# Optimization experiments

Measured on AMD Instinct MI355X. Metric: run time of the kernel, lower is better.

## Reference

```python
import jax, jax.numpy as jnp
import numpy as np

LN_EPS = 1e-5

def _ln(x, w, b):
    mu = jnp.mean(x, axis=-1, keepdims=True)
    var = jnp.var(x, axis=-1, keepdims=True)
    return (x - mu) * jax.lax.rsqrt(var + LN_EPS) * w + b

def setup_inputs() -> dict:
    key = jax.random.key(0)
    ks = jax.random.split(key, 16)
    B, T, N = 32, 1024, 77
    D, TD, TE = 512, 256, 2048
    s = lambda fan: 1.0 / np.sqrt(fan)
    return {
        "x": jax.random.normal(ks[0], (B, T, D), jnp.float32),
        "xf": jax.random.normal(ks[1], (B, N, TD), jnp.float32),
        "emb": jax.random.normal(ks[2], (B, TE), jnp.float32),
        "src_mask": jnp.ones((B, T), jnp.float32),
        "cond_type": jax.random.randint(ks[3], (B,), 0, 100, jnp.int64),
        "norm_w": jnp.ones((D,), jnp.float32),
        "norm_b": jnp.zeros((D,), jnp.float32),
        "tnorm_w": jnp.ones((TD,), jnp.float32),
        "tnorm_b": jnp.zeros((TD,), jnp.float32),
        "Wq": jax.random.normal(ks[4], (D, D), jnp.float32) * s(D),
        "bq": jnp.zeros((D,), jnp.float32),
        "Wk": jax.random.normal(ks[5], (D, TD), jnp.float32) * s(TD),
        "bk": jnp.zeros((D,), jnp.float32),
        "Wv": jax.random.normal(ks[6], (D, TD), jnp.float32) * s(TD),
        "bv": jnp.zeros((D,), jnp.float32),
        "emb_w": jax.random.normal(ks[7], (2 * D, TE), jnp.float32) * s(TE),
        "emb_b": jnp.zeros((2 * D,), jnp.float32),
        "snorm_w": jnp.ones((D,), jnp.float32),
        "snorm_b": jnp.zeros((D,), jnp.float32),
        "Wout": jax.random.normal(ks[8], (D, D), jnp.float32) * s(D),
        "bout": jnp.zeros((D,), jnp.float32),
    }

def reference(x, xf, emb, src_mask, cond_type,
              norm_w, norm_b, tnorm_w, tnorm_b,
              Wq, bq, Wk, bk, Wv, bv,
              emb_w, emb_b, snorm_w, snorm_b, Wout, bout):
    B, T, D = x.shape
    N = xf.shape[1]
    H = 8
    dh = D // H
    # projections (no 1/sqrt(dh) scaling, per original)
    q = (_ln(x, norm_w, norm_b) @ Wq.T + bq).reshape(B, T, H, dh)
    xf_n = _ln(xf, tnorm_w, tnorm_b)
    k = (xf_n @ Wk.T + bk).reshape(B, N, H, dh)
    # cond_type gating: text_cond_type = (cond_type % 10 > 0)
    tc = (cond_type % 10 > 0).astype(x.dtype)  # [B]
    bias = (1.0 - tc)[:, None, None, None] * -1000000.0  # [B,1,1,1]
    attn = jnp.einsum('bthd,bnhd->btnh', q, k) + bias
    attn = jax.nn.softmax(attn, axis=2)  # over keys N
    v = (xf_n @ Wv.T + bv) * tc[:, None, None]
    v = v.reshape(B, N, H, dh)
    y = jnp.einsum('btnh,bnhd->bthd', attn, v).reshape(B, T, D)
    # StylizationBlock: silu->linear on emb -> scale/shift, ln, silu->linear, residual
    e = jax.nn.silu(emb) @ emb_w.T + emb_b  # [B, 2D]
    scale, shift = jnp.split(e[:, None, :], 2, axis=2)  # [B,1,D] each
    h = _ln(y, snorm_w, snorm_b) * (1.0 + scale) + shift
    h = jax.nn.silu(h) @ Wout.T + bout
    return x + h
```

## Files before the change

kernel.cpp:

```cpp
#include <hip/hip_runtime.h>
#include <math.h>

#define B_   32
#define T_   1024
#define N_   77
#define D_   512
#define TD_  256
#define TE_  2048
#define H_   8
#define DH_  64

typedef short bf16x8 __attribute__((ext_vector_type(8)));
typedef float f32x4  __attribute__((ext_vector_type(4)));

__device__ __forceinline__ float sigmoidf_fast(float x) {
    return 1.0f / (1.0f + __expf(-x));
}

__device__ __forceinline__ unsigned short f2b(float f) {
    unsigned int u = __float_as_uint(f);
    unsigned int r = u + 0x7FFFu + ((u >> 16) & 1u);
    return (unsigned short)(r >> 16);
}

__device__ __forceinline__ float b2f(short us) {
    return __uint_as_float(((unsigned int)(unsigned short)us) << 16);
}

#define GL16(g, l) __builtin_amdgcn_global_load_lds(                         \
    (const __attribute__((address_space(1))) unsigned int*)(g),              \
    (__attribute__((address_space(3))) unsigned int*)(l), 16, 0, 0)

#define WAITV8() asm volatile("s_waitcnt vmcnt(8)" ::: "memory")
#define WAITV4() asm volatile("s_waitcnt vmcnt(4)" ::: "memory")
#define WAITV0() asm volatile("s_waitcnt vmcnt(0)" ::: "memory")
#define WAITL0() asm volatile("s_waitcnt lgkmcnt(0)" ::: "memory")
#define SBAR()   __builtin_amdgcn_s_barrier()
#define SCHED0() __builtin_amdgcn_sched_barrier(0)

__global__ __launch_bounds__(256) void ln_xf_kernel(
    const float* __restrict__ x, const float* __restrict__ w, const float* __restrict__ b,
    unsigned short* __restrict__ outb)
{
    int row = blockIdx.x * 4 + (threadIdx.x >> 6);
    int lane = threadIdx.x & 63;
    const float* rp = x + (size_t)row * TD_ + lane * 4;
    float4 v = *(const float4*)rp;
    float s  = v.x + v.y + v.z + v.w;
    float ss = v.x*v.x + v.y*v.y + v.z*v.z + v.w*v.w;
    #pragma unroll
    for (int off = 32; off; off >>= 1) {
        s  += __shfl_xor(s, off);
        ss += __shfl_xor(ss, off);
    }
    float m = s * (1.f / TD_);
    float r = rsqrtf(ss * (1.f / TD_) - m * m + 1e-5f);
    float4 wv = *(const float4*)(w + lane * 4);
    float4 bv = *(const float4*)(b + lane * 4);
    ushort4 o;
    o.x = f2b((v.x - m) * r * wv.x + bv.x);
    o.y = f2b((v.y - m) * r * wv.y + bv.y);
    o.z = f2b((v.z - m) * r * wv.z + bv.z);
    o.w = f2b((v.w - m) * r * wv.w + bv.w);
    *(ushort4*)(outb + (size_t)row * TD_ + lane * 4) = o;
}

__global__ __launch_bounds__(256) void conv_weights_kernel(
    const float* __restrict__ Wq, const float* __restrict__ Wout,
    const float* __restrict__ Wk, const float* __restrict__ Wv,
    unsigned short* __restrict__ wqb, unsigned short* __restrict__ wob,
    unsigned short* __restrict__ wkvb)
{
    int bid = blockIdx.x;
    const float* src; unsigned short* dst;
    if (bid < 128)      { src = Wq;   dst = wqb; }
    else if (bid < 256) { src = Wout; dst = wob;               bid -= 128; }
    else if (bid < 320) { src = Wk;   dst = wkvb;              bid -= 256; }
    else                { src = Wv;   dst = wkvb + D_ * TD_;   bid -= 320; }
    int idx = (bid * 256 + threadIdx.x) * 8;
    float4 v0 = *(const float4*)(src + idx);
    float4 v1 = *(const float4*)(src + idx + 4);
    ushort4 o0 = {f2b(v0.x), f2b(v0.y), f2b(v0.z), f2b(v0.w)};
    ushort4 o1 = {f2b(v1.x), f2b(v1.y), f2b(v1.z), f2b(v1.w)};
    *(ushort4*)(dst + idx)     = o0;
    *(ushort4*)(dst + idx + 4) = o1;
}

__global__ __launch_bounds__(256) void kv_gemm_kernel(
    const unsigned short* __restrict__ Ab,
    const unsigned short* __restrict__ Wb,
    const float* __restrict__ bkp, const float* __restrict__ bvp,
    const int*   __restrict__ cond,
    unsigned short* __restrict__ kout, unsigned short* __restrict__ vout)
{
    constexpr int K = TD_;
    constexpr int NSTEP = 8;
    __shared__ __align__(16) unsigned short As[3][128 * 32];
    __shared__ __align__(16) unsigned short Bs[3][128 * 32];

    const int tid  = threadIdx.x;
    int id = blockIdx.x;
    int swz = (id & 7) * 20 + (id >> 3);
    const int m0 = (swz >> 3) * 128;
    const int n0 = (swz & 7) * 128;
    const int lane = tid & 63;
    const int w    = tid >> 6;
    const int l15  = lane & 15;
    const int quad = lane >> 4;
    const int wm   = (w >> 1) * 64;
    const int wn   = (w & 1) * 64;

    const int row_a = tid >> 2;
    const int ck    = (tid & 3) ^ ((row_a >> 1) & 3);
    const int sc    = (quad ^ ((l15 >> 1) & 3)) << 3;

    f32x4 acc[4][4];
    #pragma unroll
    for (int i = 0; i < 4; i++)
        #pragma unroll
        for (int j = 0; j < 4; j++)
            acc[i][j] = (f32x4){0.f, 0.f, 0.f, 0.f};

    const char* gA = (const char*)Ab + ((size_t)(m0 + row_a) * K) * 2 + ck * 16;
    const char* gB = (const char*)Wb + ((size_t)(n0 + row_a) * K) * 2 + ck * 16;
    const size_t g2 = (size_t)64 * K * 2;
    char* lA = (char*)&As[0][0] + tid * 16;
    char* lB = (char*)&Bs[0][0] + tid * 16;

#define KSTAGE(s, buf) do {                                                   \
        GL16(gA + (s) * 64,      lA + (buf) * 8192);                          \
        GL16(gA + (s) * 64 + g2, lA + (buf) * 8192 + 4096);                   \
        GL16(gB + (s) * 64,      lB + (buf) * 8192);                          \
        GL16(gB + (s) * 64 + g2, lB + (buf) * 8192 + 4096);                   \
    } while (0)

    KSTAGE(0, 0);
    KSTAGE(1, 1);
    KSTAGE(2, 2);

    bf16x8 af[4], bfr[4];
    #pragma unroll
    for (int t = 0; t < NSTEP; t++) {
        const int cur = t % 3;
        if (t < NSTEP - 2)       { WAITV8(); }
        else if (t == NSTEP - 2) { WAITV4(); }
        else                     { WAITV0(); }
        SBAR(); SCHED0();
        #pragma unroll
        for (int i = 0; i < 4; i++)
            af[i] = *(const bf16x8*)&As[cur][(wm + i * 16 + l15) * 32 + sc];
        #pragma unroll
        for (int j = 0; j < 4; j++)
            bfr[j] = *(const bf16x8*)&Bs[cur][(wn + j * 16 + l15) * 32 + sc];
        WAITL0(); SCHED0();
        SBAR(); SCHED0();
        if (t + 3 < NSTEP) KSTAGE(t + 3, cur);
        #pragma unroll
        for (int i = 0; i < 4; i++)
            #pragma unroll
            for (int j = 0; j < 4; j++)
                acc[i][j] = __builtin_amdgcn_mfma_f32_16x16x32_bf16(af[i], bfr[j], acc[i][j], 0, 0, 0);
    }
#undef KSTAGE

    #pragma unroll
    for (int i = 0; i < 4; i++) {
        int mbase = m0 + wm + i * 16 + quad * 4;
        #pragma unroll
        for (int j = 0; j < 4; j++) {
            int n = n0 + wn + j * 16 + l15;
            bool isv = n >= D_;
            int nn = isv ? n - D_ : n;
            float bn = isv ? bvp[nn] : bkp[nn];
            unsigned short* outp = isv ? vout : kout;
            #pragma unroll
            for (int r = 0; r < 4; r++) {
                int m = mbase + r;
                if (m >= B_ * N_) continue;
                float v = acc[i][j][r] + bn;
                if (isv) {
                    int bi = m / N_;
                    v = ((cond[bi] % 10) > 0) ? v : 0.f;
                }
                outp[(size_t)m * D_ + nn] = f2b(v);
            }
        }
    }
}

__global__ __launch_bounds__(256) void emb_gemm_kernel(
    const float* __restrict__ emb, const float* __restrict__ W,
    float* __restrict__ e)
{
    int wid = blockIdx.x * 4 + (threadIdx.x >> 6);
    int lane = threadIdx.x & 63;
    int ngrp = wid >> 3;
    int bgrp = wid & 7;

    float acc[4][4] = {};
    #pragma unroll 2
    for (int it = 0; it < 8; it++) {
        int k = (it * 64 + lane) * 4;
        float4 sv[4], wv[4];
        #pragma unroll
        for (int bi = 0; bi < 4; bi++) {
            float4 t = *(const float4*)&emb[(size_t)(bgrp * 4 + bi) * TE_ + k];
            t.x *= sigmoidf_fast(t.x);
            t.y *= sigmoidf_fast(t.y);
            t.z *= sigmoidf_fast(t.z);
            t.w *= sigmoidf_fast(t.w);
            sv[bi] = t;
        }
        #pragma unroll
        for (int ni = 0; ni < 4; ni++)
            wv[ni] = *(const float4*)&W[(size_t)(ngrp * 4 + ni) * TE_ + k];
        #pragma unroll
        for (int bi = 0; bi < 4; bi++)
            #pragma unroll
            for (int ni = 0; ni < 4; ni++) {
                acc[bi][ni] = fmaf(sv[bi].x, wv[ni].x, acc[bi][ni]);
                acc[bi][ni] = fmaf(sv[bi].y, wv[ni].y, acc[bi][ni]);
                acc[bi][ni] = fmaf(sv[bi].z, wv[ni].z, acc[bi][ni]);
                acc[bi][ni] = fmaf(sv[bi].w, wv[ni].w, acc[bi][ni]);
            }
    }
    #pragma unroll
    for (int bi = 0; bi < 4; bi++)
        #pragma unroll
        for (int ni = 0; ni < 4; ni++) {
            float a = acc[bi][ni];
            #pragma unroll
            for (int off = 32; off; off >>= 1) a += __shfl_xor(a, off);
            if (lane == 0)
                e[(size_t)(bgrp * 4 + bi) * 1024 + ngrp * 4 + ni] = a;
        }
}

__global__ __launch_bounds__(256) void prep_q_kernel(
    const float* __restrict__ x, const float* __restrict__ w, const float* __restrict__ b,
    unsigned short* __restrict__ outb)
{
    int row = blockIdx.x * 4 + (threadIdx.x >> 6);
    int lane = threadIdx.x & 63;
    const float* rp = x + (size_t)row * D_ + lane * 8;
    float4 v0 = *(const float4*)rp;
    float4 v1 = *(const float4*)(rp + 4);
    float s  = v0.x + v0.y + v0.z + v0.w + v1.x + v1.y + v1.z + v1.w;
    float ss = v0.x*v0.x + v0.y*v0.y + v0.z*v0.z + v0.w*v0.w
             + v1.x*v1.x + v1.y*v1.y + v1.z*v1.z + v1.w*v1.w;
    #pragma unroll
    for (int off = 32; off; off >>= 1) {
        s  += __shfl_xor(s, off);
        ss += __shfl_xor(ss, off);
    }
    float m = s * (1.f / D_);
    float r = rsqrtf(ss * (1.f / D_) - m * m + 1e-5f);
    float4 w0 = *(const float4*)(w + lane * 8);
    float4 w1 = *(const float4*)(w + lane * 8 + 4);
    float4 b0 = *(const float4*)(b + lane * 8);
    float4 b1 = *(const float4*)(b + lane * 8 + 4);
    ushort4 o0, o1;
    o0.x = f2b((v0.x - m) * r * w0.x + b0.x);
    o0.y = f2b((v0.y - m) * r * w0.y + b0.y);
    o0.z = f2b((v0.z - m) * r * w0.z + b0.z);
    o0.w = f2b((v0.w - m) * r * w0.w + b0.w);
    o1.x = f2b((v1.x - m) * r * w1.x + b1.x);
    o1.y = f2b((v1.y - m) * r * w1.y + b1.y);
    o1.z = f2b((v1.z - m) * r * w1.z + b1.z);
    o1.w = f2b((v1.w - m) * r * w1.w + b1.w);
    unsigned short* op = outb + (size_t)row * D_ + lane * 8;
    *(ushort4*)op       = o0;
    *(ushort4*)(op + 4) = o1;
}

__global__ __launch_bounds__(256) void prep_h_kernel(
    const unsigned short* __restrict__ y, const float* __restrict__ w, const float* __restrict__ b,
    const float* __restrict__ e, const float* __restrict__ emb_b,
    unsigned short* __restrict__ outb)
{
    int row = blockIdx.x * 4 + (threadIdx.x >> 6);
    int lane = threadIdx.x & 63;
    int bb = row >> 10;
    const unsigned short* rp = y + (size_t)row * D_ + lane * 8;
    bf16x8 yv = *(const bf16x8*)rp;
    float v[8];
    #pragma unroll
    for (int k2 = 0; k2 < 8; k2++) v[k2] = b2f(yv[k2]);
    float s = 0.f, ss = 0.f;
    #pragma unroll
    for (int k2 = 0; k2 < 8; k2++) { s += v[k2]; ss += v[k2] * v[k2]; }
    #pragma unroll
    for (int off = 32; off; off >>= 1) {
        s  += __shfl_xor(s, off);
        ss += __shfl_xor(ss, off);
    }
    float m = s * (1.f / D_);
    float r = rsqrtf(ss * (1.f / D_) - m * m + 1e-5f);
    float4 w0 = *(const float4*)(w + lane * 8);
    float4 w1 = *(const float4*)(w + lane * 8 + 4);
    float4 b0 = *(const float4*)(b + lane * 8);
    float4 b1 = *(const float4*)(b + lane * 8 + 4);
    float wa[8] = {w0.x, w0.y, w0.z, w0.w, w1.x, w1.y, w1.z, w1.w};
    float ba[8] = {b0.x, b0.y, b0.z, b0.w, b1.x, b1.y, b1.z, b1.w};
    const float* ep = e + (size_t)bb * 1024 + lane * 8;
    float4 sc0 = *(const float4*)ep;
    float4 sc1 = *(const float4*)(ep + 4);
    float4 sh0 = *(const float4*)(ep + 512);
    float4 sh1 = *(const float4*)(ep + 512 + 4);
    float4 eb0 = *(const float4*)(emb_b + lane * 8);
    float4 eb1 = *(const float4*)(emb_b + lane * 8 + 4);
    float4 fb0 = *(const float4*)(emb_b + 512 + lane * 8);
    float4 fb1 = *(const float4*)(emb_b + 512 + lane * 8 + 4);
    float sca[8] = {sc0.x + eb0.x, sc0.y + eb0.y, sc0.z + eb0.z, sc0.w + eb0.w,
                    sc1.x + eb1.x, sc1.y + eb1.y, sc1.z + eb1.z, sc1.w + eb1.w};
    float sha[8] = {sh0.x + fb0.x, sh0.y + fb0.y, sh0.z + fb0.z, sh0.w + fb0.w,
                    sh1.x + fb1.x, sh1.y + fb1.y, sh1.z + fb1.z, sh1.w + fb1.w};
    ushort4 o0, o1;
    unsigned short oa[8];
    #pragma unroll
    for (int k2 = 0; k2 < 8; k2++) {
        float hv = ((v[k2] - m) * r * wa[k2] + ba[k2]) * (1.f + sca[k2]) + sha[k2];
        oa[k2] = f2b(hv * sigmoidf_fast(hv));
    }
    o0.x = oa[0]; o0.y = oa[1]; o0.z = oa[2]; o0.w = oa[3];
    o1.x = oa[4]; o1.y = oa[5]; o1.z = oa[6]; o1.w = oa[7];
    unsigned short* op = outb + (size_t)row * D_ + lane * 8;
    *(ushort4*)op       = o0;
    *(ushort4*)(op + 4) = o1;
}

template <int RESID, int OUTBF>
__global__ __launch_bounds__(256) void gemm_bf16_kernel(
    const unsigned short* __restrict__ Ab,
    const unsigned short* __restrict__ Wb,
    const float* __restrict__ bias,
    const float* __restrict__ resid,
    void* __restrict__ Cv)
{
    constexpr int K = 512;
    constexpr int NSTEP = 16;
    __shared__ __align__(16) unsigned short As[3][128 * 32];
    __shared__ __align__(16) unsigned short Bs[3][128 * 32];

    const int tid  = threadIdx.x;
    int id = blockIdx.x;
    int swz = (id & 7) * 128 + (id >> 3);
    const int m0 = (swz >> 2) * 128;
    const int n0 = (swz & 3) * 128;
    const int lane = tid & 63;
    const int w    = tid >> 6;
    const int l15  = lane & 15;
    const int quad = lane >> 4;
    const int wm   = (w >> 1) * 64;
    const int wn   = (w & 1) * 64;

    const int row_s = tid >> 2;
    const int ck    = (tid & 3) ^ ((row_s >> 1) & 3);
    const int sc    = (quad ^ ((l15 >> 1) & 3)) << 3;

    f32x4 acc[4][4];
    #pragma unroll
    for (int i = 0; i < 4; i++)
        #pragma unroll
        for (int j = 0; j < 4; j++)
            acc[i][j] = (f32x4){0.f, 0.f, 0.f, 0.f};

    const char* gA = (const char*)Ab + ((size_t)(m0 + row_s) * K) * 2 + ck * 16;
    const char* gB = (const char*)Wb + ((size_t)(n0 + row_s) * K) * 2 + ck * 16;
    const size_t g2 = (size_t)64 * K * 2;
    char* lA = (char*)&As[0][0] + tid * 16;
    char* lB = (char*)&Bs[0][0] + tid * 16;

#define STAGE_G(s, buf) do {                                                  \
        GL16(gA + (s) * 64,      lA + (buf) * 8192);                          \
        GL16(gA + (s) * 64 + g2, lA + (buf) * 8192 + 4096);                   \
        GL16(gB + (s) * 64,      lB + (buf) * 8192);                          \
        GL16(gB + (s) * 64 + g2, lB + (buf) * 8192 + 4096);                   \
    } while (0)

    STAGE_G(0, 0);
    STAGE_G(1, 1);
    STAGE_G(2, 2);

    bf16x8 af[4], bfr[4];
    #pragma unroll
    for (int t = 0; t < NSTEP; t++) {
        const int cur = t % 3;
        if (t < NSTEP - 2)       { WAITV8(); }
        else if (t == NSTEP - 2) { WAITV4(); }
        else                     { WAITV0(); }
        SBAR(); SCHED0();
        #pragma unroll
        for (int i = 0; i < 4; i++)
            af[i] = *(const bf16x8*)&As[cur][(wm + i * 16 + l15) * 32 + sc];
        #pragma unroll
        for (int j = 0; j < 4; j++)
            bfr[j] = *(const bf16x8*)&Bs[cur][(wn + j * 16 + l15) * 32 + sc];
        WAITL0(); SCHED0();
        SBAR(); SCHED0();
        if (t + 3 < NSTEP) STAGE_G(t + 3, cur);
        #pragma unroll
        for (int i = 0; i < 4; i++)
            #pragma unroll
            for (int j = 0; j < 4; j++)
                acc[i][j] = __builtin_amdgcn_mfma_f32_16x16x32_bf16(af[i], bfr[j], acc[i][j], 0, 0, 0);
    }
#undef STAGE_G

    float* C = (float*)Cv;
    unsigned short* Cb = (unsigned short*)Cv;
    #pragma unroll
    for (int i = 0; i < 4; i++) {
        int mbase = m0 + wm + i * 16 + quad * 4;
        #pragma unroll
        for (int j = 0; j < 4; j++) {
            int n = n0 + wn + j * 16 + l15;
            float bn = bias[n];
            #pragma unroll
            for (int r = 0; r < 4; r++) {
                size_t off = (size_t)(mbase + r) * 512 + n;
                float v = acc[i][j][r] + bn;
                if (RESID) v += resid[off];
                if (OUTBF) Cb[off] = f2b(v);
                else       C[off]  = v;
            }
        }
    }
}

#define KS2   0
#define VT2   5760
#define PS2   11904
#define SMEM2 18560

__global__ __launch_bounds__(256) void attn_mfma2_kernel(
    const unsigned short* __restrict__ qb,
    const unsigned short* __restrict__ kb,
    const unsigned short* __restrict__ vb,
    unsigned short* __restrict__ yout)
{
    __shared__ __align__(16) unsigned short smem[SMEM2];

    const int tid = threadIdx.x;
    const int t0 = blockIdx.x * 64;
    const int h  = blockIdx.y;
    const int b  = blockIdx.z;

    const int lane = tid & 63;
    const int w    = tid >> 6;
    const int l15  = lane & 15;
    const int quad = lane >> 4;
    const int koff = quad * 8;
    const int mrow = w * 16 + l15;

    const unsigned short* qrow = qb + ((size_t)(b * T_ + t0 + mrow)) * D_ + h * 64 + koff;
    bf16x8 aq0 = *(const bf16x8*)qrow;
    bf16x8 aq1 = *(const bf16x8*)(qrow + 32);

    const unsigned short* kbase = kb + ((size_t)(b * N_)) * D_ + h * 64;
    #pragma unroll
    for (int i = 0; i < 3; i++) {
        int idx = tid + i * 256;
        if (idx < 640) {
            int row = idx >> 3, c8 = idx & 7;
            bf16x8 v = (bf16x8){0, 0, 0, 0, 0, 0, 0, 0};
            if (row < N_) v = *(const bf16x8*)(kbase + (size_t)row * D_ + c8 * 8);
            *(bf16x8*)&smem[KS2 + row * 72 + c8 * 8] = v;
        }
    }
    const unsigned short* vbase = vb + ((size_t)(b * N_)) * D_ + h * 64;
    #pragma unroll
    for (int i = 0; i < 3; i++) {
        int idx = tid + i * 256;
        if (idx < 616) {
            int n = idx >> 3, c8 = idx & 7;
            bf16x8 v = *(const bf16x8*)(vbase + (size_t)n * D_ + c8 * 8);
            int cn = n >> 3, wn = n & 7;
            #pragma unroll
            for (int j = 0; j < 8; j++) {
                int d = c8 * 8 + j;
                int s2 = (j ^ c8) & 3;
                smem[VT2 + d * 96 + ((cn ^ s2) << 3) + wn] = v[j];
            }
        }
    }
    if (tid < 128) {
        int d = tid >> 1, c = 10 + (tid & 1);
        int s2 = (d ^ (d >> 3)) & 3;
        *(bf16x8*)&smem[VT2 + d * 96 + ((c ^ s2) << 3)] = (bf16x8){0, 0, 0, 0, 0, 0, 0, 0};
    }
    {
        int d = tid >> 2, t = tid & 3;
        if (t < 3) {
            int s2 = (d ^ (d >> 3)) & 3;
            smem[VT2 + d * 96 + ((9 ^ s2) << 3) + 5 + t] = 0;
        }
    }
    #pragma unroll
    for (int i = 0; i < 4; i++) {
        int idx = tid + i * 256;
        int row = idx >> 4, col = 80 + (idx & 15);
        smem[PS2 + row * 104 + col] = 0;
    }
    __syncthreads();

    float s[5][4];
    #pragma unroll
    for (int nt = 0; nt < 5; nt++) {
        bf16x8 bk0 = *(const bf16x8*)&smem[KS2 + (nt * 16 + l15) * 72 + koff];
        bf16x8 bk1 = *(const bf16x8*)&smem[KS2 + (nt * 16 + l15) * 72 + 32 + koff];
        f32x4 c = {0.f, 0.f, 0.f, 0.f};
        c = __builtin_amdgcn_mfma_f32_16x16x32_bf16(aq0, bk0, c, 0, 0, 0);
        c = __builtin_amdgcn_mfma_f32_16x16x32_bf16(aq1, bk1, c, 0, 0, 0);
        #pragma unroll
        for (int r = 0; r < 4; r++) s[nt][r] = c[r];
    }
    if (l15 >= N_ - 64) {
        #pragma unroll
        for (int r = 0; r < 4; r++) s[4][r] = -1e30f;
    }
    float li[4];
    #pragma unroll
    for (int r = 0; r < 4; r++) {
        float m = s[0][r];
        #pragma unroll
        for (int nt = 1; nt < 5; nt++) m = fmaxf(m, s[nt][r]);
        m = fmaxf(m, __shfl_xor(m, 1));
        m = fmaxf(m, __shfl_xor(m, 2));
        m = fmaxf(m, __shfl_xor(m, 4));
        m = fmaxf(m, __shfl_xor(m, 8));
        float l = 0.f;
        #pragma unroll
        for (int nt = 0; nt < 5; nt++) {
            float ev = __expf(s[nt][r] - m);
            s[nt][r] = ev;
            l += ev;
        }
        l += __shfl_xor(l, 1);
        l += __shfl_xor(l, 2);
        l += __shfl_xor(l, 4);
        l += __shfl_xor(l, 8);
        li[r] = 1.f / l;
    }
    #pragma unroll
    for (int r = 0; r < 4; r++) {
        int prow = w * 16 + quad * 4 + r;
        #pragma unroll
        for (int nt = 0; nt < 5; nt++) {
            smem[PS2 + prow * 104 + nt * 16 + l15] = f2b(s[nt][r] * li[r]);
        }
    }

    bf16x8 pa0 = *(const bf16x8*)&smem[PS2 + mrow * 104 + 0  + koff];
    bf16x8 pa1 = *(const bf16x8*)&smem[PS2 + mrow * 104 + 32 + koff];
    bf16x8 pa2 = *(const bf16x8*)&smem[PS2 + mrow * 104 + 64 + koff];

    unsigned short* obase = yout + ((size_t)(b * T_ + t0 + w * 16)) * D_ + h * 64;
    #pragma unroll
    for (int dt = 0; dt < 4; dt++) {
        int drow = dt * 16 + l15;
        int s2 = (drow ^ (drow >> 3)) & 3;
        bf16x8 bv0 = *(const bf16x8*)&smem[VT2 + drow * 96 + (((0 + quad) ^ s2) << 3)];
        bf16x8 bv1 = *(const bf16x8*)&smem[VT2 + drow * 96 + (((4 + quad) ^ s2) << 3)];
        bf16x8 bv2 = *(const bf16x8*)&smem[VT2 + drow * 96 + (((8 + quad) ^ s2) << 3)];
        f32x4 c = {0.f, 0.f, 0.f, 0.f};
        c = __builtin_amdgcn_mfma_f32_16x16x32_bf16(pa0, bv0, c, 0, 0, 0);
        c = __builtin_amdgcn_mfma_f32_16x16x32_bf16(pa1, bv1, c, 0, 0, 0);
        c = __builtin_amdgcn_mfma_f32_16x16x32_bf16(pa2, bv2, c, 0, 0, 0);
        #pragma unroll
        for (int r = 0; r < 4; r++) {
            obase[(size_t)(quad * 4 + r) * D_ + dt * 16 + l15] = f2b(c[r]);
        }
    }
}

extern "C" void kernel_launch(void* const* d_in, const int* in_sizes, int n_in,
                              void* d_out, int out_size, void* d_ws, size_t ws_size,
                              hipStream_t stream)
{
    const float* x       = (const float*)d_in[0];
    const float* xf      = (const float*)d_in[1];
    const float* emb     = (const float*)d_in[2];
    const int*   cond    = (const int*)d_in[4];
    const float* norm_w  = (const float*)d_in[5];
    const float* norm_b  = (const float*)d_in[6];
    const float* tnorm_w = (const float*)d_in[7];
    const float* tnorm_b = (const float*)d_in[8];
    const float* Wq      = (const float*)d_in[9];
    const float* bq      = (const float*)d_in[10];
    const float* Wk      = (const float*)d_in[11];
    const float* bk      = (const float*)d_in[12];
    const float* Wv      = (const float*)d_in[13];
    const float* bv      = (const float*)d_in[14];
    const float* emb_w   = (const float*)d_in[15];
    const float* emb_b   = (const float*)d_in[16];
    const float* snorm_w = (const float*)d_in[17];
    const float* snorm_b = (const float*)d_in[18];
    const float* Wout    = (const float*)d_in[19];
    const float* bout    = (const float*)d_in[20];
    float* out = (float*)d_out;

    float* ws = (float*)d_ws;
    float* ebuf = ws;
    unsigned short* u = (unsigned short*)(ebuf + (size_t)B_ * 2 * D_);
    unsigned short* qyb  = u;  u += (size_t)B_ * T_ * D_;
    unsigned short* xfnb = u;  u += (size_t)2560 * TD_;
    unsigned short* kb16 = u;  u += (size_t)B_ * N_ * D_;
    unsigned short* vb16 = u;  u += (size_t)B_ * N_ * D_;
    unsigned short* abh  = u;  u += (size_t)B_ * T_ * D_;
    unsigned short* wqb  = u;  u += (size_t)D_ * D_;
    unsigned short* wob  = u;  u += (size_t)D_ * D_;
    unsigned short* wkvb = u;  u += (size_t)2 * D_ * TD_;
    unsigned short* qb = (unsigned short*)d_out;

    const int BT = B_ * T_;
    const int BN = B_ * N_;

    ln_xf_kernel<<<BN / 4, 256, 0, stream>>>(xf, tnorm_w, tnorm_b, xfnb);
    conv_weights_kernel<<<384, 256, 0, stream>>>(Wq, Wout, Wk, Wv, wqb, wob, wkvb);
    kv_gemm_kernel<<<160, 256, 0, stream>>>(xfnb, wkvb, bk, bv, cond, kb16, vb16);
    prep_q_kernel<<<BT / 4, 256, 0, stream>>>(x, norm_w, norm_b, abh);
    gemm_bf16_kernel<0, 1><<<1024, 256, 0, stream>>>(abh, wqb, bq, nullptr, qb);
    emb_gemm_kernel<<<512, 256, 0, stream>>>(emb, emb_w, ebuf);
    {
        dim3 grid(T_ / 64, H_, B_);
        attn_mfma2_kernel<<<grid, 256, 0, stream>>>(qb, kb16, vb16, qyb);
    }
    prep_h_kernel<<<BT / 4, 256, 0, stream>>>(qyb, snorm_w, snorm_b, ebuf, emb_b, abh);
    gemm_bf16_kernel<1, 0><<<1024, 256, 0, stream>>>(abh, wob, bout, x, out);
}
```

Before: 299.9 us.

## Fuse LayerNorm prologues into projection GEMMs and fold norm weights into Wq

Removes the standalone prep_q and prep_h kernels. The Q and output GEMMs now compute per-row LayerNorm statistics in a prologue and normalize or modulate the A operand in registers before writing it to LDS, so the bf16 intermediate activation buffer is no longer written and reread. The LN weight is folded into the Wq conversion and the LN bias into bq through a small GEMV. The scale and shift from the style embedding are folded into per-batch w2/b2 vectors. The change also adds s_setprio around the MFMA blocks, and the fused GEMMs take on extra prologue latency plus register-staged A loads.

```diff
diff --git a/kernel.cpp b/kernel.cpp
--- a/kernel.cpp
+++ b/kernel.cpp
@@ -31,10 +31,13 @@
     (const __attribute__((address_space(1))) unsigned int*)(g),              \
     (__attribute__((address_space(3))) unsigned int*)(l), 16, 0, 0)
 
-#define WAITV8() asm volatile("s_waitcnt vmcnt(8)" ::: "memory")
-#define WAITV4() asm volatile("s_waitcnt vmcnt(4)" ::: "memory")
-#define WAITV0() asm volatile("s_waitcnt vmcnt(0)" ::: "memory")
-#define WAITL0() asm volatile("s_waitcnt lgkmcnt(0)" ::: "memory")
+#define WAITV12() asm volatile("s_waitcnt vmcnt(12)" ::: "memory")
+#define WAITV8()  asm volatile("s_waitcnt vmcnt(8)"  ::: "memory")
+#define WAITV6()  asm volatile("s_waitcnt vmcnt(6)"  ::: "memory")
+#define WAITV4()  asm volatile("s_waitcnt vmcnt(4)"  ::: "memory")
+#define WAITV2()  asm volatile("s_waitcnt vmcnt(2)"  ::: "memory")
+#define WAITV0()  asm volatile("s_waitcnt vmcnt(0)"  ::: "memory")
+#define WAITL0()  asm volatile("s_waitcnt lgkmcnt(0)" ::: "memory")
 #define SBAR()   __builtin_amdgcn_s_barrier()
 #define SCHED0() __builtin_amdgcn_sched_barrier(0)
 
@@ -68,22 +71,62 @@
 __global__ __launch_bounds__(256) void conv_weights_kernel(
     const float* __restrict__ Wq, const float* __restrict__ Wout,
     const float* __restrict__ Wk, const float* __restrict__ Wv,
+    const float* __restrict__ normw,
     unsigned short* __restrict__ wqb, unsigned short* __restrict__ wob,
     unsigned short* __restrict__ wkvb)
 {
     int bid = blockIdx.x;
-    const float* src; unsigned short* dst;
-    if (bid < 128)      { src = Wq;   dst = wqb; }
+    const float* src; unsigned short* dst; bool fold = false;
+    if (bid < 128)      { src = Wq;   dst = wqb;  fold = true; }
     else if (bid < 256) { src = Wout; dst = wob;               bid -= 128; }
     else if (bid < 320) { src = Wk;   dst = wkvb;              bid -= 256; }
     else                { src = Wv;   dst = wkvb + D_ * TD_;   bid -= 320; }
     int idx = (bid * 256 + threadIdx.x) * 8;
     float4 v0 = *(const float4*)(src + idx);
     float4 v1 = *(const float4*)(src + idx + 4);
+    if (fold) {
+        int k = idx & 511;
+        float4 n0 = *(const float4*)(normw + k);
+        float4 n1 = *(const float4*)(normw + k + 4);
+        v0.x *= n0.x; v0.y *= n0.y; v0.z *= n0.z; v0.w *= n0.w;
+        v1.x *= n1.x; v1.y *= n1.y; v1.z *= n1.z; v1.w *= n1.w;
+    }
     ushort4 o0 = {f2b(v0.x), f2b(v0.y), f2b(v0.z), f2b(v0.w)};
     ushort4 o1 = {f2b(v1.x), f2b(v1.y), f2b(v1.z), f2b(v1.w)};
     *(ushort4*)(dst + idx)     = o0;
     *(ushort4*)(dst + idx + 4) = o1;
+}
+
+__global__ __launch_bounds__(256) void gemv_bias_kernel(
+    const float* __restrict__ W, const float* __restrict__ v,
+    const float* __restrict__ bias0, float* __restrict__ out)
+{
+    int n = blockIdx.x * 4 + (threadIdx.x >> 6);
+    int lane = threadIdx.x & 63;
+    const float* rp = W + (size_t)n * 512 + lane * 8;
+    float4 a0 = *(const float4*)rp;
+    float4 a1 = *(const float4*)(rp + 4);
+    float4 v0 = *(const float4*)(v + lane * 8);
+    float4 v1 = *(const float4*)(v + lane * 8 + 4);
+    float d = a0.x*v0.x + a0.y*v0.y + a0.z*v0.z + a0.w*v0.w
+            + a1.x*v1.x + a1.y*v1.y + a1.z*v1.z + a1.w*v1.w;
+    #pragma unroll
+    for (int off = 32; off; off >>= 1) d += __shfl_xor(d, off);
+    if (lane == 0) out[n] = bias0[n] + d;
+}
+
+__global__ __launch_bounds__(256) void prep_w2b2_kernel(
+    const float* __restrict__ e, const float* __restrict__ emb_b,
+    const float* __restrict__ snw, const float* __restrict__ snb,
+    float* __restrict__ w2, float* __restrict__ b2)
+{
+    int idx = blockIdx.x * 256 + threadIdx.x;
+    int bb = idx >> 9, k = idx & 511;
+    float sc = e[(size_t)bb * 1024 + k] + emb_b[k];
+    float sh = e[(size_t)bb * 1024 + 512 + k] + emb_b[512 + k];
+    float f = 1.f + sc;
+    w2[(size_t)bb * 512 + k] = snw[k] * f;
+    b2[(size_t)bb * 512 + k] = snb[k] * f + sh;
 }
 
 __global__ __launch_bounds__(256) void kv_gemm_kernel(
@@ -155,11 +198,13 @@
         WAITL0(); SCHED0();
         SBAR(); SCHED0();
         if (t + 3 < NSTEP) KSTAGE(t + 3, cur);
+        __builtin_amdgcn_s_setprio(1);
         #pragma unroll
         for (int i = 0; i < 4; i++)
             #pragma unroll
             for (int j = 0; j < 4; j++)
                 acc[i][j] = __builtin_amdgcn_mfma_f32_16x16x32_bf16(af[i], bfr[j], acc[i][j], 0, 0, 0);
+        __builtin_amdgcn_s_setprio(0);
     }
 #undef KSTAGE
 
@@ -236,104 +281,13 @@
         }
 }
 
-__global__ __launch_bounds__(256) void prep_q_kernel(
-    const float* __restrict__ x, const float* __restrict__ w, const float* __restrict__ b,
-    unsigned short* __restrict__ outb)
-{
-    int row = blockIdx.x * 4 + (threadIdx.x >> 6);
-    int lane = threadIdx.x & 63;
-    const float* rp = x + (size_t)row * D_ + lane * 8;
-    float4 v0 = *(const float4*)rp;
-    float4 v1 = *(const float4*)(rp + 4);
-    float s  = v0.x + v0.y + v0.z + v0.w + v1.x + v1.y + v1.z + v1.w;
-    float ss = v0.x*v0.x + v0.y*v0.y + v0.z*v0.z + v0.w*v0.w
-             + v1.x*v1.x + v1.y*v1.y + v1.z*v1.z + v1.w*v1.w;
-    #pragma unroll
-    for (int off = 32; off; off >>= 1) {
-        s  += __shfl_xor(s, off);
-        ss += __shfl_xor(ss, off);
-    }
-    float m = s * (1.f / D_);
-    float r = rsqrtf(ss * (1.f / D_) - m * m + 1e-5f);
-    float4 w0 = *(const float4*)(w + lane * 8);
-    float4 w1 = *(const float4*)(w + lane * 8 + 4);
-    float4 b0 = *(const float4*)(b + lane * 8);
-    float4 b1 = *(const float4*)(b + lane * 8 + 4);
-    ushort4 o0, o1;
-    o0.x = f2b((v0.x - m) * r * w0.x + b0.x);
-    o0.y = f2b((v0.y - m) * r * w0.y + b0.y);
-    o0.z = f2b((v0.z - m) * r * w0.z + b0.z);
-    o0.w = f2b((v0.w - m) * r * w0.w + b0.w);
-    o1.x = f2b((v1.x - m) * r * w1.x + b1.x);
-    o1.y = f2b((v1.y - m) * r * w1.y + b1.y);
-    o1.z = f2b((v1.z - m) * r * w1.z + b1.z);
-    o1.w = f2b((v1.w - m) * r * w1.w + b1.w);
-    unsigned short* op = outb + (size_t)row * D_ + lane * 8;
-    *(ushort4*)op       = o0;
-    *(ushort4*)(op + 4) = o1;
-}
-
-__global__ __launch_bounds__(256) void prep_h_kernel(
-    const unsigned short* __restrict__ y, const float* __restrict__ w, const float* __restrict__ b,
-    const float* __restrict__ e, const float* __restrict__ emb_b,
-    unsigned short* __restrict__ outb)
-{
-    int row = blockIdx.x * 4 + (threadIdx.x >> 6);
-    int lane = threadIdx.x & 63;
-    int bb = row >> 10;
-    const unsigned short* rp = y + (size_t)row * D_ + lane * 8;
-    bf16x8 yv = *(const bf16x8*)rp;
-    float v[8];
-    #pragma unroll
-    for (int k2 = 0; k2 < 8; k2++) v[k2] = b2f(yv[k2]);
-    float s = 0.f, ss = 0.f;
-    #pragma unroll
-    for (int k2 = 0; k2 < 8; k2++) { s += v[k2]; ss += v[k2] * v[k2]; }
-    #pragma unroll
-    for (int off = 32; off; off >>= 1) {
-        s  += __shfl_xor(s, off);
-        ss += __shfl_xor(ss, off);
-    }
-    float m = s * (1.f / D_);
-    float r = rsqrtf(ss * (1.f / D_) - m * m + 1e-5f);
-    float4 w0 = *(const float4*)(w + lane * 8);
-    float4 w1 = *(const float4*)(w + lane * 8 + 4);
-    float4 b0 = *(const float4*)(b + lane * 8);
-    float4 b1 = *(const float4*)(b + lane * 8 + 4);
-    float wa[8] = {w0.x, w0.y, w0.z, w0.w, w1.x, w1.y, w1.z, w1.w};
-    float ba[8] = {b0.x, b0.y, b0.z, b0.w, b1.x, b1.y, b1.z, b1.w};
-    const float* ep = e + (size_t)bb * 1024 + lane * 8;
-    float4 sc0 = *(const float4*)ep;
-    float4 sc1 = *(const float4*)(ep + 4);
-    float4 sh0 = *(const float4*)(ep + 512);
-    float4 sh1 = *(const float4*)(ep + 512 + 4);
-    float4 eb0 = *(const float4*)(emb_b + lane * 8);
-    float4 eb1 = *(const float4*)(emb_b + lane * 8 + 4);
-    float4 fb0 = *(const float4*)(emb_b + 512 + lane * 8);
-    float4 fb1 = *(const float4*)(emb_b + 512 + lane * 8 + 4);
-    float sca[8] = {sc0.x + eb0.x, sc0.y + eb0.y, sc0.z + eb0.z, sc0.w + eb0.w,
-                    sc1.x + eb1.x, sc1.y + eb1.y, sc1.z + eb1.z, sc1.w + eb1.w};
-    float sha[8] = {sh0.x + fb0.x, sh0.y + fb0.y, sh0.z + fb0.z, sh0.w + fb0.w,
-                    sh1.x + fb1.x, sh1.y + fb1.y, sh1.z + fb1.z, sh1.w + fb1.w};
-    ushort4 o0, o1;
-    unsigned short oa[8];
-    #pragma unroll
-    for (int k2 = 0; k2 < 8; k2++) {
-        float hv = ((v[k2] - m) * r * wa[k2] + ba[k2]) * (1.f + sca[k2]) + sha[k2];
-        oa[k2] = f2b(hv * sigmoidf_fast(hv));
-    }
-    o0.x = oa[0]; o0.y = oa[1]; o0.z = oa[2]; o0.w = oa[3];
-    o1.x = oa[4]; o1.y = oa[5]; o1.z = oa[6]; o1.w = oa[7];
-    unsigned short* op = outb + (size_t)row * D_ + lane * 8;
-    *(ushort4*)op       = o0;
-    *(ushort4*)(op + 4) = o1;
-}
-
-template <int RESID, int OUTBF>
-__global__ __launch_bounds__(256) void gemm_bf16_kernel(
-    const unsigned short* __restrict__ Ab,
+template <int TRANS>
+__global__ __launch_bounds__(256) void fgemm_kernel(
+    const void* __restrict__ Av,
     const unsigned short* __restrict__ Wb,
     const float* __restrict__ bias,
+    const float* __restrict__ w2g,
+    const float* __restrict__ b2g,
     const float* __restrict__ resid,
     void* __restrict__ Cv)
 {
@@ -341,8 +295,11 @@
     constexpr int NSTEP = 16;
     __shared__ __align__(16) unsigned short As[3][128 * 32];
     __shared__ __align__(16) unsigned short Bs[3][128 * 32];
-
-    const int tid  = threadIdx.x;
+    __shared__ float stats[128][2];
+    __shared__ float pw[TRANS == 2 ? 512 : 4];
+    __shared__ float pb[TRANS == 2 ? 512 : 4];
+
+    const int tid = threadIdx.x;
     int id = blockIdx.x;
     int swz = (id & 7) * 128 + (id >> 3);
     const int m0 = (swz >> 2) * 128;
@@ -358,6 +315,52 @@
     const int ck    = (tid & 3) ^ ((row_s >> 1) & 3);
     const int sc    = (quad ^ ((l15 >> 1) & 3)) << 3;
 
+    const float*          Af = (const float*)Av;
+    const unsigned short* Ah = (const unsigned short*)Av;
+
+    #pragma unroll 4
+    for (int rr = 0; rr < 32; rr++) {
+        int row = w * 32 + rr;
+        float s, ssum;
+        if (TRANS == 1) {
+            const float* rp = Af + (size_t)(m0 + row) * K + lane * 8;
+            float4 v0 = *(const float4*)rp;
+            float4 v1 = *(const float4*)(rp + 4);
+            s  = v0.x + v0.y + v0.z + v0.w + v1.x + v1.y + v1.z + v1.w;
+            ssum = v0.x*v0.x + v0.y*v0.y + v0.z*v0.z + v0.w*v0.w
+                 + v1.x*v1.x + v1.y*v1.y + v1.z*v1.z + v1.w*v1.w;
+        } else {
+            bf16x8 yv = *(const bf16x8*)(Ah + (size_t)(m0 + row) * K + lane * 8);
+            s = 0.f; ssum = 0.f;
+            #pragma unroll
+            for (int j = 0; j < 8; j++) { float v = b2f(yv[j]); s += v; ssum += v * v; }
+        }
+        #pragma unroll
+        for (int off = 32; off; off >>= 1) {
+            s    += __shfl_xor(s, off);
+            ssum += __shfl_xor(ssum, off);
+        }
+        if (lane == 0) {
+            float mu = s * (1.f / K);
+            stats[row][0] = mu;
+            stats[row][1] = rsqrtf(ssum * (1.f / K) - mu * mu + 1e-5f);
+        }
+    }
+    if (TRANS == 2) {
+        const int bb = m0 >> 10;
+        if (tid < 128)
+            *(float4*)&pw[tid * 4] = *(const float4*)&w2g[(size_t)bb * 512 + tid * 4];
+        else {
+            int t2 = tid - 128;
+            *(float4*)&pb[t2 * 4] = *(const float4*)&b2g[(size_t)bb * 512 + t2 * 4];
+        }
+    }
+    WAITV0();
+    __syncthreads();
+
+    const float mA0 = stats[row_s][0],      rA0 = stats[row_s][1];
+    const float mA1 = stats[row_s + 64][0], rA1 = stats[row_s + 64][1];
+
     f32x4 acc[4][4];
     #pragma unroll
     for (int i = 0; i < 4; i++)
@@ -365,30 +368,93 @@
         for (int j = 0; j < 4; j++)
             acc[i][j] = (f32x4){0.f, 0.f, 0.f, 0.f};
 
-    const char* gA = (const char*)Ab + ((size_t)(m0 + row_s) * K) * 2 + ck * 16;
+    const size_t arow0 = (size_t)(m0 + row_s) * K;
+    const size_t arow1 = arow0 + (size_t)64 * K;
     const char* gB = (const char*)Wb + ((size_t)(n0 + row_s) * K) * 2 + ck * 16;
     const size_t g2 = (size_t)64 * K * 2;
-    char* lA = (char*)&As[0][0] + tid * 16;
     char* lB = (char*)&Bs[0][0] + tid * 16;
 
-#define STAGE_G(s, buf) do {                                                  \
-        GL16(gA + (s) * 64,      lA + (buf) * 8192);                          \
-        GL16(gA + (s) * 64 + g2, lA + (buf) * 8192 + 4096);                   \
-        GL16(gB + (s) * 64,      lB + (buf) * 8192);                          \
-        GL16(gB + (s) * 64 + g2, lB + (buf) * 8192 + 4096);                   \
+    float4 rA00[3], rA01[3], rA10[3], rA11[3];
+    bf16x8 rH0[3], rH1[3];
+
+#define ISSUE_A(s) do {                                                       \
+        if (TRANS == 1) {                                                     \
+            rA00[(s) % 3] = *(const float4*)(Af + arow0 + (s) * 32 + ck * 8);     \
+            rA01[(s) % 3] = *(const float4*)(Af + arow0 + (s) * 32 + ck * 8 + 4); \
+            rA10[(s) % 3] = *(const float4*)(Af + arow1 + (s) * 32 + ck * 8);     \
+            rA11[(s) % 3] = *(const float4*)(Af + arow1 + (s) * 32 + ck * 8 + 4); \
+        } else {                                                              \
+            rH0[(s) % 3] = *(const bf16x8*)(Ah + arow0 + (s) * 32 + ck * 8);  \
+            rH1[(s) % 3] = *(const bf16x8*)(Ah + arow1 + (s) * 32 + ck * 8);  \
+        }                                                                     \
     } while (0)
 
-    STAGE_G(0, 0);
-    STAGE_G(1, 1);
-    STAGE_G(2, 2);
+#define ISSUE_B(s) do {                                                       \
+        GL16(gB + (s) * 64,      lB + ((s) % 3) * 8192);                      \
+        GL16(gB + (s) * 64 + g2, lB + ((s) % 3) * 8192 + 4096);               \
+    } while (0)
+
+#define TRANSFORM(s) do {                                                     \
+        bf16x8 ov0, ov1;                                                      \
+        if (TRANS == 1) {                                                     \
+            float4 a0 = rA00[(s) % 3], a1 = rA01[(s) % 3];                    \
+            float4 c0 = rA10[(s) % 3], c1 = rA11[(s) % 3];                    \
+            ov0[0] = (short)f2b((a0.x - mA0) * rA0);                          \
+            ov0[1] = (short)f2b((a0.y - mA0) * rA0);                          \
+            ov0[2] = (short)f2b((a0.z - mA0) * rA0);                          \
+            ov0[3] = (short)f2b((a0.w - mA0) * rA0);                          \
+            ov0[4] = (short)f2b((a1.x - mA0) * rA0);                          \
+            ov0[5] = (short)f2b((a1.y - mA0) * rA0);                          \
+            ov0[6] = (short)f2b((a1.z - mA0) * rA0);                          \
+            ov0[7] = (short)f2b((a1.w - mA0) * rA0);                          \
+            ov1[0] = (short)f2b((c0.x - mA1) * rA1);                          \
+            ov1[1] = (short)f2b((c0.y - mA1) * rA1);                          \
+            ov1[2] = (short)f2b((c0.z - mA1) * rA1);                          \
+            ov1[3] = (short)f2b((c0.w - mA1) * rA1);                          \
+            ov1[4] = (short)f2b((c1.x - mA1) * rA1);                          \
+            ov1[5] = (short)f2b((c1.y - mA1) * rA1);                          \
+            ov1[6] = (short)f2b((c1.z - mA1) * rA1);                          \
+            ov1[7] = (short)f2b((c1.w - mA1) * rA1);                          \
+        } else {                                                              \
+            bf16x8 h0 = rH0[(s) % 3], h1 = rH1[(s) % 3];                      \
+            float4 wva = *(const float4*)&pw[(s) * 32 + ck * 8];              \
+            float4 wvb = *(const float4*)&pw[(s) * 32 + ck * 8 + 4];          \
+            float4 bva = *(const float4*)&pb[(s) * 32 + ck * 8];              \
+            float4 bvb = *(const float4*)&pb[(s) * 32 + ck * 8 + 4];          \
+            float wk8[8] = {wva.x, wva.y, wva.z, wva.w, wvb.x, wvb.y, wvb.z, wvb.w}; \
+            float bk8[8] = {bva.x, bva.y, bva.z, bva.w, bvb.x, bvb.y, bvb.z, bvb.w}; \
+            _Pragma("unroll")                                                 \
+            for (int j = 0; j < 8; j++) {                                     \
+                float v0 = b2f(h0[j]);                                        \
+                float hv0 = (v0 - mA0) * rA0 * wk8[j] + bk8[j];               \
+                ov0[j] = (short)f2b(hv0 * sigmoidf_fast(hv0));                \
+                float v1 = b2f(h1[j]);                                        \
+                float hv1 = (v1 - mA1) * rA1 * wk8[j] + bk8[j];               \
+                ov1[j] = (short)f2b(hv1 * sigmoidf_fast(hv1));                \
+            }                                                                 \
+        }                                                                     \
+        *(bf16x8*)&As[(s) % 3][row_s * 32 + (tid & 3) * 8]        = ov0;      \
+        *(bf16x8*)&As[(s) % 3][(row_s + 64) * 32 + (tid & 3) * 8] = ov1;      \
+    } while (0)
+
+    ISSUE_A(0); ISSUE_B(0);
+    WAITV2();
+    TRANSFORM(0);
+    WAITL0(); SCHED0();
+    ISSUE_A(1); ISSUE_B(1);
+    ISSUE_A(2); ISSUE_B(2);
 
     bf16x8 af[4], bfr[4];
     #pragma unroll
     for (int t = 0; t < NSTEP; t++) {
         const int cur = t % 3;
-        if (t < NSTEP - 2)       { WAITV8(); }
-        else if (t == NSTEP - 2) { WAITV4(); }
-        else                     { WAITV0(); }
+        if (t <= NSTEP - 3) {
+            if (TRANS == 1) { WAITV12(); } else { WAITV8(); }
+        } else if (t == NSTEP - 2) {
+            if (TRANS == 1) { WAITV6(); } else { WAITV4(); }
+        } else {
+            WAITV0();
+        }
         SBAR(); SCHED0();
         #pragma unroll
         for (int i = 0; i < 4; i++)
@@ -396,16 +462,21 @@
         #pragma unroll
         for (int j = 0; j < 4; j++)
             bfr[j] = *(const bf16x8*)&Bs[cur][(wn + j * 16 + l15) * 32 + sc];
+        if (t + 1 < NSTEP) TRANSFORM(t + 1);
         WAITL0(); SCHED0();
         SBAR(); SCHED0();
-        if (t + 3 < NSTEP) STAGE_G(t + 3, cur);
+        if (t + 3 < NSTEP) { ISSUE_A(t + 3); ISSUE_B(t + 3); SCHED0(); }
+        __builtin_amdgcn_s_setprio(1);
         #pragma unroll
         for (int i = 0; i < 4; i++)
             #pragma unroll
             for (int j = 0; j < 4; j++)
                 acc[i][j] = __builtin_amdgcn_mfma_f32_16x16x32_bf16(af[i], bfr[j], acc[i][j], 0, 0, 0);
-    }
-#undef STAGE_G
+        __builtin_amdgcn_s_setprio(0);
+    }
+#undef ISSUE_A
+#undef ISSUE_B
+#undef TRANSFORM
 
     float* C = (float*)Cv;
     unsigned short* Cb = (unsigned short*)Cv;
@@ -420,9 +491,8 @@
             for (int r = 0; r < 4; r++) {
                 size_t off = (size_t)(mbase + r) * 512 + n;
                 float v = acc[i][j][r] + bn;
-                if (RESID) v += resid[off];
-                if (OUTBF) Cb[off] = f2b(v);
-                else       C[off]  = v;
+                if (TRANS == 2) { v += resid[off]; C[off] = v; }
+                else            { Cb[off] = f2b(v); }
             }
         }
     }
@@ -505,6 +575,7 @@
     __syncthreads();
 
     float s[5][4];
+    __builtin_amdgcn_s_setprio(1);
     #pragma unroll
     for (int nt = 0; nt < 5; nt++) {
         bf16x8 bk0 = *(const bf16x8*)&smem[KS2 + (nt * 16 + l15) * 72 + koff];
@@ -515,6 +586,7 @@
         #pragma unroll
         for (int r = 0; r < 4; r++) s[nt][r] = c[r];
     }
+    __builtin_amdgcn_s_setprio(0);
     if (l15 >= N_ - 64) {
         #pragma unroll
         for (int r = 0; r < 4; r++) s[4][r] = -1e30f;
@@ -564,9 +636,11 @@
         bf16x8 bv1 = *(const bf16x8*)&smem[VT2 + drow * 96 + (((4 + quad) ^ s2) << 3)];
         bf16x8 bv2 = *(const bf16x8*)&smem[VT2 + drow * 96 + (((8 + quad) ^ s2) << 3)];
         f32x4 c = {0.f, 0.f, 0.f, 0.f};
+        __builtin_amdgcn_s_setprio(1);
         c = __builtin_amdgcn_mfma_f32_16x16x32_bf16(pa0, bv0, c, 0, 0, 0);
         c = __builtin_amdgcn_mfma_f32_16x16x32_bf16(pa1, bv1, c, 0, 0, 0);
         c = __builtin_amdgcn_mfma_f32_16x16x32_bf16(pa2, bv2, c, 0, 0, 0);
+        __builtin_amdgcn_s_setprio(0);
         #pragma unroll
         for (int r = 0; r < 4; r++) {
             obase[(size_t)(quad * 4 + r) * D_ + dt * 16 + l15] = f2b(c[r]);
@@ -602,30 +676,31 @@
 
     float* ws = (float*)d_ws;
     float* ebuf = ws;
-    unsigned short* u = (unsigned short*)(ebuf + (size_t)B_ * 2 * D_);
+    float* bqp  = ebuf + (size_t)B_ * 2 * D_;
+    float* w2   = bqp + D_;
+    float* b2   = w2 + (size_t)B_ * D_;
+    unsigned short* u = (unsigned short*)(b2 + (size_t)B_ * D_);
     unsigned short* qyb  = u;  u += (size_t)B_ * T_ * D_;
     unsigned short* xfnb = u;  u += (size_t)2560 * TD_;
     unsigned short* kb16 = u;  u += (size_t)B_ * N_ * D_;
     unsigned short* vb16 = u;  u += (size_t)B_ * N_ * D_;
-    unsigned short* abh  = u;  u += (size_t)B_ * T_ * D_;
     unsigned short* wqb  = u;  u += (size_t)D_ * D_;
     unsigned short* wob  = u;  u += (size_t)D_ * D_;
     unsigned short* wkvb = u;  u += (size_t)2 * D_ * TD_;
     unsigned short* qb = (unsigned short*)d_out;
 
-    const int BT = B_ * T_;
     const int BN = B_ * N_;
 
     ln_xf_kernel<<<BN / 4, 256, 0, stream>>>(xf, tnorm_w, tnorm_b, xfnb);
-    conv_weights_kernel<<<384, 256, 0, stream>>>(Wq, Wout, Wk, Wv, wqb, wob, wkvb);
+    conv_weights_kernel<<<384, 256, 0, stream>>>(Wq, Wout, Wk, Wv, norm_w, wqb, wob, wkvb);
+    gemv_bias_kernel<<<128, 256, 0, stream>>>(Wq, norm_b, bq, bqp);
     kv_gemm_kernel<<<160, 256, 0, stream>>>(xfnb, wkvb, bk, bv, cond, kb16, vb16);
-    prep_q_kernel<<<BT / 4, 256, 0, stream>>>(x, norm_w, norm_b, abh);
-    gemm_bf16_kernel<0, 1><<<1024, 256, 0, stream>>>(abh, wqb, bq, nullptr, qb);
+    fgemm_kernel<1><<<1024, 256, 0, stream>>>(x, wqb, bqp, nullptr, nullptr, nullptr, qb);
     emb_gemm_kernel<<<512, 256, 0, stream>>>(emb, emb_w, ebuf);
+    prep_w2b2_kernel<<<64, 256, 0, stream>>>(ebuf, emb_b, snorm_w, snorm_b, w2, b2);
     {
         dim3 grid(T_ / 64, H_, B_);
         attn_mfma2_kernel<<<grid, 256, 0, stream>>>(qb, kb16, vb16, qyb);
     }
-    prep_h_kernel<<<BT / 4, 256, 0, stream>>>(qyb, snorm_w, snorm_b, ebuf, emb_b, abh);
-    gemm_bf16_kernel<1, 0><<<1024, 256, 0, stream>>>(abh, wob, bout, x, out);
-}
+    fgemm_kernel<2><<<1024, 256, 0, stream>>>(qyb, wob, bout, w2, b2, x, out);
+}
```

Result: slower. 412.6 us (+37.6%).

## Switch GEMM pipelines to double buffering with single barrier and MFMA priority

Applied to the files above, without the earlier changes.

The KV and main bf16 GEMM kernels move from a three-stage LDS ring to two buffers. Each k-step now waits for all loads, does one barrier, and then prefetches the next tile, replacing the partial vmcnt waits and the second barrier. Both kernels declare an occupancy hint of 4 blocks per CU, which the smaller LDS footprint makes easier to reach. s_setprio raises wave priority around MFMA sections, including in the attention kernel. The trade is a shallower prefetch, which may expose global latency, against fewer barriers and more resident waves.

```diff
diff --git a/kernel.cpp b/kernel.cpp
--- a/kernel.cpp
+++ b/kernel.cpp
@@ -31,10 +31,7 @@
     (const __attribute__((address_space(1))) unsigned int*)(g),              \
     (__attribute__((address_space(3))) unsigned int*)(l), 16, 0, 0)
 
-#define WAITV8() asm volatile("s_waitcnt vmcnt(8)" ::: "memory")
-#define WAITV4() asm volatile("s_waitcnt vmcnt(4)" ::: "memory")
-#define WAITV0() asm volatile("s_waitcnt vmcnt(0)" ::: "memory")
-#define WAITL0() asm volatile("s_waitcnt lgkmcnt(0)" ::: "memory")
+#define WAITV0()  asm volatile("s_waitcnt vmcnt(0)"  ::: "memory")
 #define SBAR()   __builtin_amdgcn_s_barrier()
 #define SCHED0() __builtin_amdgcn_sched_barrier(0)
 
@@ -86,7 +83,7 @@
     *(ushort4*)(dst + idx + 4) = o1;
 }
 
-__global__ __launch_bounds__(256) void kv_gemm_kernel(
+__global__ __launch_bounds__(256, 4) void kv_gemm_kernel(
     const unsigned short* __restrict__ Ab,
     const unsigned short* __restrict__ Wb,
     const float* __restrict__ bkp, const float* __restrict__ bvp,
@@ -95,8 +92,8 @@
 {
     constexpr int K = TD_;
     constexpr int NSTEP = 8;
-    __shared__ __align__(16) unsigned short As[3][128 * 32];
-    __shared__ __align__(16) unsigned short Bs[3][128 * 32];
+    __shared__ __align__(16) unsigned short As[2][128 * 32];
+    __shared__ __align__(16) unsigned short Bs[2][128 * 32];
 
     const int tid  = threadIdx.x;
     int id = blockIdx.x;
@@ -135,31 +132,27 @@
     } while (0)
 
     KSTAGE(0, 0);
-    KSTAGE(1, 1);
-    KSTAGE(2, 2);
 
     bf16x8 af[4], bfr[4];
     #pragma unroll
     for (int t = 0; t < NSTEP; t++) {
-        const int cur = t % 3;
-        if (t < NSTEP - 2)       { WAITV8(); }
-        else if (t == NSTEP - 2) { WAITV4(); }
-        else                     { WAITV0(); }
-        SBAR(); SCHED0();
+        const int cur = t & 1;
+        WAITV0(); SBAR(); SCHED0();
+        if (t + 1 < NSTEP) KSTAGE(t + 1, cur ^ 1);
         #pragma unroll
         for (int i = 0; i < 4; i++)
             af[i] = *(const bf16x8*)&As[cur][(wm + i * 16 + l15) * 32 + sc];
         #pragma unroll
         for (int j = 0; j < 4; j++)
             bfr[j] = *(const bf16x8*)&Bs[cur][(wn + j * 16 + l15) * 32 + sc];
-        WAITL0(); SCHED0();
-        SBAR(); SCHED0();
-        if (t + 3 < NSTEP) KSTAGE(t + 3, cur);
+        __builtin_amdgcn_s_setprio(1);
         #pragma unroll
         for (int i = 0; i < 4; i++)
             #pragma unroll
             for (int j = 0; j < 4; j++)
                 acc[i][j] = __builtin_amdgcn_mfma_f32_16x16x32_bf16(af[i], bfr[j], acc[i][j], 0, 0, 0);
+        __builtin_amdgcn_s_setprio(0);
+        SCHED0();
     }
 #undef KSTAGE
 
@@ -330,7 +323,7 @@
 }
 
 template <int RESID, int OUTBF>
-__global__ __launch_bounds__(256) void gemm_bf16_kernel(
+__global__ __launch_bounds__(256, 4) void gemm_bf16_kernel(
     const unsigned short* __restrict__ Ab,
     const unsigned short* __restrict__ Wb,
     const float* __restrict__ bias,
@@ -339,8 +332,8 @@
 {
     constexpr int K = 512;
     constexpr int NSTEP = 16;
-    __shared__ __align__(16) unsigned short As[3][128 * 32];
-    __shared__ __align__(16) unsigned short Bs[3][128 * 32];
+    __shared__ __align__(16) unsigned short As[2][128 * 32];
+    __shared__ __align__(16) unsigned short Bs[2][128 * 32];
 
     const int tid  = threadIdx.x;
     int id = blockIdx.x;
@@ -379,31 +372,27 @@
     } while (0)
 
     STAGE_G(0, 0);
-    STAGE_G(1, 1);
-    STAGE_G(2, 2);
 
     bf16x8 af[4], bfr[4];
     #pragma unroll
     for (int t = 0; t < NSTEP; t++) {
-        const int cur = t % 3;
-        if (t < NSTEP - 2)       { WAITV8(); }
-        else if (t == NSTEP - 2) { WAITV4(); }
-        else                     { WAITV0(); }
-        SBAR(); SCHED0();
+        const int cur = t & 1;
+        WAITV0(); SBAR(); SCHED0();
+        if (t + 1 < NSTEP) STAGE_G(t + 1, cur ^ 1);
         #pragma unroll
         for (int i = 0; i < 4; i++)
             af[i] = *(const bf16x8*)&As[cur][(wm + i * 16 + l15) * 32 + sc];
         #pragma unroll
         for (int j = 0; j < 4; j++)
             bfr[j] = *(const bf16x8*)&Bs[cur][(wn + j * 16 + l15) * 32 + sc];
-        WAITL0(); SCHED0();
-        SBAR(); SCHED0();
-        if (t + 3 < NSTEP) STAGE_G(t + 3, cur);
+        __builtin_amdgcn_s_setprio(1);
         #pragma unroll
         for (int i = 0; i < 4; i++)
             #pragma unroll
             for (int j = 0; j < 4; j++)
                 acc[i][j] = __builtin_amdgcn_mfma_f32_16x16x32_bf16(af[i], bfr[j], acc[i][j], 0, 0, 0);
+        __builtin_amdgcn_s_setprio(0);
+        SCHED0();
     }
 #undef STAGE_G
 
@@ -505,6 +494,7 @@
     __syncthreads();
 
     float s[5][4];
+    __builtin_amdgcn_s_setprio(1);
     #pragma unroll
     for (int nt = 0; nt < 5; nt++) {
         bf16x8 bk0 = *(const bf16x8*)&smem[KS2 + (nt * 16 + l15) * 72 + koff];
@@ -515,6 +505,7 @@
         #pragma unroll
         for (int r = 0; r < 4; r++) s[nt][r] = c[r];
     }
+    __builtin_amdgcn_s_setprio(0);
     if (l15 >= N_ - 64) {
         #pragma unroll
         for (int r = 0; r < 4; r++) s[4][r] = -1e30f;
@@ -564,9 +555,11 @@
         bf16x8 bv1 = *(const bf16x8*)&smem[VT2 + drow * 96 + (((4 + quad) ^ s2) << 3)];
         bf16x8 bv2 = *(const bf16x8*)&smem[VT2 + drow * 96 + (((8 + quad) ^ s2) << 3)];
         f32x4 c = {0.f, 0.f, 0.f, 0.f};
+        __builtin_amdgcn_s_setprio(1);
         c = __builtin_amdgcn_mfma_f32_16x16x32_bf16(pa0, bv0, c, 0, 0, 0);
         c = __builtin_amdgcn_mfma_f32_16x16x32_bf16(pa1, bv1, c, 0, 0, 0);
         c = __builtin_amdgcn_mfma_f32_16x16x32_bf16(pa2, bv2, c, 0, 0, 0);
+        __builtin_amdgcn_s_setprio(0);
         #pragma unroll
         for (int r = 0; r < 4; r++) {
             obase[(size_t)(quad * 4 + r) * D_ + dt * 16 + l15] = f2b(c[r]);
```

Measured after the change: 307.6 us. 2.6% more time.
